# Performance work log

Measured on AMD Instinct MI355X. Metric: run time of the kernel, lower is better.

Reference implementation:

```python
import jax, jax.numpy as jnp
import numpy as np

TOTAL = 262144
NUM_SEG = 1024
H_DIM = 64
BF = 2  # block_flag_num
EPS = 1e-5


def setup_inputs() -> dict:
    key = jax.random.key(0)
    ks = jax.random.split(key, 12)
    # equal-length contiguous segments (ragged in general; equal here for setup)
    bounds = np.arange(0, TOTAL + 1, TOTAL // NUM_SEG, dtype=np.int64)
    seq_start_end = jnp.asarray(np.stack([bounds[:-1], bounds[1:]], axis=1))
    d_in = BF * 2          # 4
    d_emb = BF * 16        # 32
    d_pre = d_emb + H_DIM  # 96
    s = lambda n: 1.0 / np.sqrt(n)
    return {
        'h_state': jax.random.normal(ks[0], (TOTAL, H_DIM), jnp.float32),
        'end_block_pos_rel': jax.random.normal(ks[1], (TOTAL, 2, BF), jnp.float32),
        'W_sp': jax.random.normal(ks[2], (d_emb, d_in), jnp.float32) * s(d_in),
        'b_sp': jnp.zeros((d_emb,), jnp.float32),
        'W1': jax.random.normal(ks[3], (512, d_pre), jnp.float32) * s(d_pre),
        'b1': jnp.zeros((512,), jnp.float32),
        'g1': jnp.ones((512,), jnp.float32),
        'be1': jnp.zeros((512,), jnp.float32),
        'W2': jax.random.normal(ks[4], (1024, 512), jnp.float32) * s(512),
        'b2': jnp.zeros((1024,), jnp.float32),
        'g2': jnp.ones((1024,), jnp.float32),
        'be2': jnp.zeros((1024,), jnp.float32),
        'seq_start_end': seq_start_end,
    }


def _segment_bn(x, seg_ids, counts, gamma, beta):
    # training-mode BatchNorm1d computed independently per segment (biased var)
    num_seg = counts.shape[0]
    mean = jax.ops.segment_sum(x, seg_ids, num_segments=num_seg) / counts[:, None]
    ex2 = jax.ops.segment_sum(x * x, seg_ids, num_segments=num_seg) / counts[:, None]
    var = ex2 - mean * mean
    xn = (x - mean[seg_ids]) * jax.lax.rsqrt(var[seg_ids] + EPS)
    return xn * gamma + beta


def reference(h_state, end_block_pos_rel, W_sp, b_sp, W1, b1, g1, be1, W2, b2, g2, be2, seq_start_end):
    total = h_state.shape[0]
    starts = seq_start_end[:, 0]
    # contiguous segments: segment id of each row
    seg_ids = jnp.searchsorted(starts, jnp.arange(total), side='right') - 1
    counts = (seq_start_end[:, 1] - seq_start_end[:, 0]).astype(h_state.dtype)
    # permute(0,2,1).view(n,-1): (total, 2, BF) -> (total, BF*2)
    pos = jnp.transpose(end_block_pos_rel, (0, 2, 1)).reshape(total, -1)
    rel_emb = pos @ W_sp.T + b_sp                              # (total, 32)
    mlp_in = jnp.concatenate([rel_emb, h_state], axis=1)       # (total, 96)
    h1 = jax.nn.relu(_segment_bn(mlp_in @ W1.T + b1, seg_ids, counts, g1, be1))
    out = jax.nn.relu(_segment_bn(h1 @ W2.T + b2, seg_ids, counts, g2, be2))
    return out  # (total, 1024)
```

## Files before the change

kernel.cpp:

```cpp
#include <hip/hip_runtime.h>
#include <hip/hip_bf16.h>

#define TOTALROWS 262144
#define NSEG      1024
#define SEGROWS   256
#define HD        64
#define DEMB      32
#define DPRE      96
#define N1        512
#define N2        1024
#define EPSB      1e-5f

typedef short s16x8 __attribute__((ext_vector_type(8)));
typedef float f32x4 __attribute__((ext_vector_type(4)));

static __device__ __forceinline__ ushort f2bf(float x) {
    union { float f; unsigned u; } v; v.f = x;
    unsigned r = v.u + 0x7FFFu + ((v.u >> 16) & 1u);
    return (ushort)(r >> 16);
}

static __device__ __forceinline__ void gload_lds16(const void* g, void* l) {
    __builtin_amdgcn_global_load_lds(
        (const __attribute__((address_space(1))) void*)g,
        (__attribute__((address_space(3))) void*)l, 16, 0, 0);
}

__global__ void convert_w2_kernel(const float* __restrict__ w2, ushort* __restrict__ w2b) {
    int i = blockIdx.x * 256 + threadIdx.x;
    float4 v = ((const float4*)w2)[i];
    ushort4 o;
    o.x = f2bf(v.x); o.y = f2bf(v.y); o.z = f2bf(v.z); o.w = f2bf(v.w);
    ((ushort4*)w2b)[i] = o;
}

__global__ __launch_bounds__(512, 2) void layer1_kernel(
    const float* __restrict__ hstate, const float* __restrict__ ebpr,
    const float* __restrict__ Wsp, const float* __restrict__ W1,
    const float* __restrict__ g1, const float* __restrict__ be1,
    ushort* __restrict__ h1)
{
    __shared__ __align__(16) ushort As[SEGROWS * 104];
    __shared__ __align__(16) ushort Bs[SEGROWS * 104];
    __shared__ float statsS[8][4][16];
    __shared__ float statsQ[8][4][16];

    const int seg  = blockIdx.x;
    const int ct   = blockIdx.y;
    const int tid  = threadIdx.x;
    const int lane = tid & 63, wid = tid >> 6;
    const int wr   = wid >> 2, wc = wid & 3;

    {
        const float4* hs4 = (const float4*)(hstate + (size_t)seg * SEGROWS * HD);
        #pragma unroll
        for (int i = 0; i < 8; ++i) {
            int u = tid + i * 512;
            int r = u >> 4, c4 = u & 15;
            float4 v = hs4[u];
            ushort* dst = &As[r * 104 + DEMB + c4 * 4];
            dst[0] = f2bf(v.x); dst[1] = f2bf(v.y); dst[2] = f2bf(v.z); dst[3] = f2bf(v.w);
        }
        #pragma unroll
        for (int i = 0; i < 16; ++i) {
            int u = tid + i * 512;
            int r = u >> 5, k = u & 31;
            float4 e = ((const float4*)ebpr)[seg * SEGROWS + r];
            float4 w = ((const float4*)Wsp)[k];
            float val = w.x * e.x + w.y * e.z + w.z * e.y + w.w * e.w;
            As[r * 104 + k] = f2bf(val);
        }
    }
    {
        const float4* w14 = (const float4*)(W1 + (size_t)ct * 256 * DPRE);
        #pragma unroll
        for (int i = 0; i < 12; ++i) {
            int u = tid + i * 512;
            int r = u / 24, c4 = u % 24;
            float4 v = w14[u];
            ushort* dst = &Bs[r * 104 + c4 * 4];
            dst[0] = f2bf(v.x); dst[1] = f2bf(v.y); dst[2] = f2bf(v.z); dst[3] = f2bf(v.w);
        }
    }
    __syncthreads();

    f32x4 acc[8][4] = {};
    const int arow0 = wr * 128 + (lane & 15);
    const int bcol0 = wc * 64  + (lane & 15);
    const int kg    = (lane >> 4) * 8;
    #pragma unroll
    for (int ks = 0; ks < 3; ++ks) {
        s16x8 af[8], bfr[4];
        #pragma unroll
        for (int m = 0; m < 8; ++m)
            af[m] = *(const s16x8*)&As[(arow0 + m * 16) * 104 + ks * 32 + kg];
        #pragma unroll
        for (int n = 0; n < 4; ++n)
            bfr[n] = *(const s16x8*)&Bs[(bcol0 + n * 16) * 104 + ks * 32 + kg];
        #pragma unroll
        for (int m = 0; m < 8; ++m)
            #pragma unroll
            for (int n = 0; n < 4; ++n)
                acc[m][n] = __builtin_amdgcn_mfma_f32_16x16x32_bf16(af[m], bfr[n], acc[m][n], 0, 0, 0);
    }

    float s[4], q[4];
    #pragma unroll
    for (int n = 0; n < 4; ++n) { s[n] = 0.f; q[n] = 0.f; }
    #pragma unroll
    for (int m = 0; m < 8; ++m)
        #pragma unroll
        for (int n = 0; n < 4; ++n)
            #pragma unroll
            for (int j = 0; j < 4; ++j) { float v = acc[m][n][j]; s[n] += v; q[n] += v * v; }
    #pragma unroll
    for (int n = 0; n < 4; ++n) {
        s[n] += __shfl_xor(s[n], 16); q[n] += __shfl_xor(q[n], 16);
        s[n] += __shfl_xor(s[n], 32); q[n] += __shfl_xor(q[n], 32);
    }
    if ((lane >> 4) == 0) {
        #pragma unroll
        for (int n = 0; n < 4; ++n) { statsS[wid][n][lane] = s[n]; statsQ[wid][n][lane] = q[n]; }
    }
    __syncthreads();

    const float inv256 = 1.0f / 256.0f;
    float aa[4], bb[4];
    const int c16 = lane & 15;
    #pragma unroll
    for (int n = 0; n < 4; ++n) {
        float sum = statsS[wc][n][c16] + statsS[4 + wc][n][c16];
        float sq  = statsQ[wc][n][c16] + statsQ[4 + wc][n][c16];
        float mean = sum * inv256;
        float var  = sq * inv256 - mean * mean;
        float rinv = rsqrtf(var + EPSB);
        int col = ct * 256 + wc * 64 + n * 16 + c16;
        aa[n] = g1[col] * rinv;
        bb[n] = be1[col] - mean * aa[n];
    }

    ushort* outp = h1 + (size_t)(seg * SEGROWS) * N1 + ct * 256;
    const int rbase = wr * 128 + (lane >> 4) * 4;
    #pragma unroll
    for (int m = 0; m < 8; ++m)
        #pragma unroll
        for (int j = 0; j < 4; ++j) {
            int r = rbase + m * 16 + j;
            ushort* rowp = outp + (size_t)r * N1 + wc * 64 + c16;
            #pragma unroll
            for (int n = 0; n < 4; ++n) {
                float v = acc[m][n][j] * aa[n] + bb[n];
                v = v > 0.f ? v : 0.f;
                rowp[n * 16] = f2bf(v);
            }
        }
}


static __device__ __forceinline__ void stage_tile(
    const char* gA, const char* gB, char* lA, char* lB,
    int t, int wid, int lane)
{
    const int rsub = lane >> 2;
    const int cl   = (((lane & 3) ^ ((lane >> 3) & 3)) << 4);
    #pragma unroll
    for (int i = 0; i < 4; ++i) {
        int g = i * 4 + wid;
        gload_lds16(gA + (size_t)(g * 16 + rsub) * 1024 + (size_t)t * 64 + cl,
                    lA + g * 1024);
    }
    #pragma unroll
    for (int i = 0; i < 2; ++i) {
        int g = i * 4 + wid;
        gload_lds16(gB + (size_t)(g * 16 + rsub) * 1024 + (size_t)t * 64 + cl,
                    lB + g * 1024);
    }
}

static __device__ __forceinline__ void compute_step(
    const ushort* lA, const ushort* lB, f32x4 (&acc)[8][4],
    int arow0, int bcol0, int swz)
{
    s16x8 af[8], bfr[4];
    #pragma unroll
    for (int m = 0; m < 8; ++m)
        af[m] = *(const s16x8*)&lA[(arow0 + m * 16) * 32 + swz];
    #pragma unroll
    for (int n = 0; n < 4; ++n)
        bfr[n] = *(const s16x8*)&lB[(bcol0 + n * 16) * 32 + swz];
    __builtin_amdgcn_s_setprio(1);
    #pragma unroll
    for (int m = 0; m < 8; ++m)
        #pragma unroll
        for (int n = 0; n < 4; ++n)
            acc[m][n] = __builtin_amdgcn_mfma_f32_16x16x32_bf16(af[m], bfr[n], acc[m][n], 0, 0, 0);
    __builtin_amdgcn_s_setprio(0);
}

__global__ __launch_bounds__(256, 2) void layer2_kernel(
    const ushort* __restrict__ h1, const ushort* __restrict__ W2b,
    const float* __restrict__ g2, const float* __restrict__ be2,
    float* __restrict__ out)
{
    __shared__ __align__(16) ushort As[3][SEGROWS * 32];
    __shared__ __align__(16) ushort Bs[3][128 * 32];
    __shared__ float statsS[4][4][16];
    __shared__ float statsQ[4][4][16];

    const int b   = blockIdx.x;
    const int wg  = (b & 7) * 1024 + (b >> 3);
    const int seg = wg >> 3;
    const int ct  = wg & 7;

    const int tid  = threadIdx.x;
    const int lane = tid & 63, wid = tid >> 6;
    const int wr   = wid >> 1, wc = wid & 1;

    const char* srcA = (const char*)(h1  + (size_t)seg * SEGROWS * N1);
    const char* srcB = (const char*)(W2b + (size_t)ct  * 128    * N1);

    f32x4 acc[8][4] = {};
    const int arow0 = wr * 128 + (lane & 15);
    const int bcol0 = wc * 64  + (lane & 15);
    const int swz  = (((lane >> 4) ^ ((lane >> 1) & 3)) << 3);

    stage_tile(srcA, srcB, (char*)As[0], (char*)Bs[0], 0, wid, lane);
    stage_tile(srcA, srcB, (char*)As[1], (char*)Bs[1], 1, wid, lane);

#define L2_STEP(T, VW)                                                              \
    {                                                                               \
        if ((T) + 2 < 16)                                                           \
            stage_tile(srcA, srcB, (char*)As[((T)+2)%3], (char*)Bs[((T)+2)%3],      \
                       (T)+2, wid, lane);                                           \
        asm volatile("s_waitcnt vmcnt(" #VW ")" ::: "memory");                      \
        __builtin_amdgcn_s_barrier();                                               \
        compute_step(As[(T)%3], Bs[(T)%3], acc, arow0, bcol0, swz);                 \
        __builtin_amdgcn_s_barrier();                                               \
    }

    L2_STEP(0, 12)  L2_STEP(1, 12)  L2_STEP(2, 12)  L2_STEP(3, 12)
    L2_STEP(4, 12)  L2_STEP(5, 12)  L2_STEP(6, 12)  L2_STEP(7, 12)
    L2_STEP(8, 12)  L2_STEP(9, 12)  L2_STEP(10, 12) L2_STEP(11, 12)
    L2_STEP(12, 12) L2_STEP(13, 12) L2_STEP(14, 6)  L2_STEP(15, 0)
#undef L2_STEP

    float s[4], q[4];
    #pragma unroll
    for (int n = 0; n < 4; ++n) { s[n] = 0.f; q[n] = 0.f; }
    #pragma unroll
    for (int m = 0; m < 8; ++m)
        #pragma unroll
        for (int n = 0; n < 4; ++n)
            #pragma unroll
            for (int j = 0; j < 4; ++j) { float v = acc[m][n][j]; s[n] += v; q[n] += v * v; }
    #pragma unroll
    for (int n = 0; n < 4; ++n) {
        s[n] += __shfl_xor(s[n], 16); q[n] += __shfl_xor(q[n], 16);
        s[n] += __shfl_xor(s[n], 32); q[n] += __shfl_xor(q[n], 32);
    }
    if ((lane >> 4) == 0) {
        #pragma unroll
        for (int n = 0; n < 4; ++n) { statsS[wid][n][lane] = s[n]; statsQ[wid][n][lane] = q[n]; }
    }
    __syncthreads();

    const float inv256 = 1.0f / 256.0f;
    float aa[4], bb[4];
    const int c16 = lane & 15;
    #pragma unroll
    for (int n = 0; n < 4; ++n) {
        float sum = statsS[wc][n][c16] + statsS[2 + wc][n][c16];
        float sq  = statsQ[wc][n][c16] + statsQ[2 + wc][n][c16];
        float mean = sum * inv256;
        float var  = sq * inv256 - mean * mean;
        float rinv = rsqrtf(var + EPSB);
        int col = ct * 128 + wc * 64 + n * 16 + c16;
        aa[n] = g2[col] * rinv;
        bb[n] = be2[col] - mean * aa[n];
    }

    float* outp = out + (size_t)(seg * SEGROWS) * N2 + ct * 128;
    const int rbase = wr * 128 + (lane >> 4) * 4;
    #pragma unroll
    for (int m = 0; m < 8; ++m)
        #pragma unroll
        for (int j = 0; j < 4; ++j) {
            int r = rbase + m * 16 + j;
            float* rowp = outp + (size_t)r * N2 + wc * 64 + c16;
            #pragma unroll
            for (int n = 0; n < 4; ++n) {
                float v = acc[m][n][j] * aa[n] + bb[n];
                v = v > 0.f ? v : 0.f;
                __builtin_nontemporal_store(v, rowp + n * 16);
            }
        }
}

extern "C" void kernel_launch(void* const* d_in, const int* in_sizes, int n_in,
                              void* d_out, int out_size, void* d_ws, size_t ws_size,
                              hipStream_t stream) {
    const float* hstate = (const float*)d_in[0];
    const float* ebpr   = (const float*)d_in[1];
    const float* Wsp    = (const float*)d_in[2];
    const float* W1     = (const float*)d_in[4];
    const float* g1     = (const float*)d_in[6];
    const float* be1    = (const float*)d_in[7];
    const float* W2     = (const float*)d_in[8];
    const float* g2     = (const float*)d_in[10];
    const float* be2    = (const float*)d_in[11];
    float* outp         = (float*)d_out;

    ushort* h1  = (ushort*)d_ws;
    ushort* W2b = h1 + (size_t)TOTALROWS * N1;

    convert_w2_kernel<<<dim3((N2 * N1 / 4) / 256), dim3(256), 0, stream>>>(W2, W2b);
    layer1_kernel<<<dim3(NSEG, 2), dim3(512), 0, stream>>>(hstate, ebpr, Wsp, W1, g1, be1, h1);
    layer2_kernel<<<dim3(8192), dim3(256), 0, stream>>>(h1, W2b, g2, be2, outp);
}
```

Measured before the change: 646.3 us.

## Retile layer2 to 256x64 double-buffered tiles and merge layer1 column tiles

Layer2 now uses 256x64 output tiles with double buffering, occupancy 3, and regular stores in place of nontemporal ones. This doubles the grid and re-reads the h1 A tile twice as often. Layer1 now runs both column tiles in one block, reusing the staged activations, and reads W1 pre-converted to bf16 by an extended conversion kernel. Its activation staging uses vectorized LDS writes. The aim is better occupancy and less conversion and staging work, at the cost of more A-operand traffic in layer2.

```diff
diff --git a/kernel.cpp b/kernel.cpp
--- a/kernel.cpp
+++ b/kernel.cpp
@@ -12,6 +12,7 @@
 #define EPSB      1e-5f
 
 typedef short s16x8 __attribute__((ext_vector_type(8)));
+typedef short s16x4 __attribute__((ext_vector_type(4)));
 typedef float f32x4 __attribute__((ext_vector_type(4)));
 
 static __device__ __forceinline__ ushort f2bf(float x) {
@@ -26,17 +27,21 @@
         (__attribute__((address_space(3))) void*)l, 16, 0, 0);
 }
 
-__global__ void convert_w2_kernel(const float* __restrict__ w2, ushort* __restrict__ w2b) {
+__global__ void convert_w_kernel(const float* __restrict__ w2, ushort* __restrict__ w2b,
+                                 const float* __restrict__ w1, ushort* __restrict__ w1b) {
     int i = blockIdx.x * 256 + threadIdx.x;
-    float4 v = ((const float4*)w2)[i];
+    const float* src; ushort* dst; int j;
+    if (i < 131072) { src = w2; dst = w2b; j = i; }
+    else            { src = w1; dst = w1b; j = i - 131072; if (j >= 12288) return; }
+    float4 v = ((const float4*)src)[j];
     ushort4 o;
     o.x = f2bf(v.x); o.y = f2bf(v.y); o.z = f2bf(v.z); o.w = f2bf(v.w);
-    ((ushort4*)w2b)[i] = o;
+    ((ushort4*)dst)[j] = o;
 }
 
 __global__ __launch_bounds__(512, 2) void layer1_kernel(
     const float* __restrict__ hstate, const float* __restrict__ ebpr,
-    const float* __restrict__ Wsp, const float* __restrict__ W1,
+    const float* __restrict__ Wsp, const ushort* __restrict__ W1b,
     const float* __restrict__ g1, const float* __restrict__ be1,
     ushort* __restrict__ h1)
 {
@@ -46,7 +51,6 @@
     __shared__ float statsQ[8][4][16];
 
     const int seg  = blockIdx.x;
-    const int ct   = blockIdx.y;
     const int tid  = threadIdx.x;
     const int lane = tid & 63, wid = tid >> 6;
     const int wr   = wid >> 2, wc = wid & 3;
@@ -54,110 +58,125 @@
     {
         const float4* hs4 = (const float4*)(hstate + (size_t)seg * SEGROWS * HD);
         #pragma unroll
-        for (int i = 0; i < 8; ++i) {
+        for (int i = 0; i < 4; ++i) {
             int u = tid + i * 512;
-            int r = u >> 4, c4 = u & 15;
-            float4 v = hs4[u];
-            ushort* dst = &As[r * 104 + DEMB + c4 * 4];
-            dst[0] = f2bf(v.x); dst[1] = f2bf(v.y); dst[2] = f2bf(v.z); dst[3] = f2bf(v.w);
-        }
-        #pragma unroll
-        for (int i = 0; i < 16; ++i) {
+            int r = u >> 3, c8 = u & 7;
+            float4 v0 = hs4[2 * u];
+            float4 v1 = hs4[2 * u + 1];
+            s16x8 o;
+            o[0] = (short)f2bf(v0.x); o[1] = (short)f2bf(v0.y);
+            o[2] = (short)f2bf(v0.z); o[3] = (short)f2bf(v0.w);
+            o[4] = (short)f2bf(v1.x); o[5] = (short)f2bf(v1.y);
+            o[6] = (short)f2bf(v1.z); o[7] = (short)f2bf(v1.w);
+            *(s16x8*)&As[r * 104 + DEMB + c8 * 8] = o;
+        }
+    }
+    {
+        #pragma unroll
+        for (int i = 0; i < 4; ++i) {
             int u = tid + i * 512;
-            int r = u >> 5, k = u & 31;
+            int r = u >> 3, kq = u & 7;
             float4 e = ((const float4*)ebpr)[seg * SEGROWS + r];
-            float4 w = ((const float4*)Wsp)[k];
-            float val = w.x * e.x + w.y * e.z + w.z * e.y + w.w * e.w;
-            As[r * 104 + k] = f2bf(val);
-        }
-    }
-    {
-        const float4* w14 = (const float4*)(W1 + (size_t)ct * 256 * DPRE);
-        #pragma unroll
-        for (int i = 0; i < 12; ++i) {
-            int u = tid + i * 512;
-            int r = u / 24, c4 = u % 24;
-            float4 v = w14[u];
-            ushort* dst = &Bs[r * 104 + c4 * 4];
-            dst[0] = f2bf(v.x); dst[1] = f2bf(v.y); dst[2] = f2bf(v.z); dst[3] = f2bf(v.w);
-        }
-    }
-    __syncthreads();
-
-    f32x4 acc[8][4] = {};
-    const int arow0 = wr * 128 + (lane & 15);
-    const int bcol0 = wc * 64  + (lane & 15);
-    const int kg    = (lane >> 4) * 8;
-    #pragma unroll
-    for (int ks = 0; ks < 3; ++ks) {
-        s16x8 af[8], bfr[4];
+            s16x4 o;
+            #pragma unroll
+            for (int t = 0; t < 4; ++t) {
+                float4 w = ((const float4*)Wsp)[kq * 4 + t];
+                float val = w.x * e.x + w.y * e.z + w.z * e.y + w.w * e.w;
+                o[t] = (short)f2bf(val);
+            }
+            *(s16x4*)&As[r * 104 + kq * 4] = o;
+        }
+    }
+
+    #pragma unroll 1
+    for (int ct = 0; ct < 2; ++ct) {
+        {
+            const s16x8* w18 = (const s16x8*)(W1b + (size_t)ct * 256 * DPRE);
+            #pragma unroll
+            for (int i = 0; i < 6; ++i) {
+                int u = tid + i * 512;
+                int r = u / 12, c8 = u % 12;
+                *(s16x8*)&Bs[r * 104 + c8 * 8] = w18[u];
+            }
+        }
+        __syncthreads();
+
+        f32x4 acc[8][4] = {};
+        const int arow0 = wr * 128 + (lane & 15);
+        const int bcol0 = wc * 64  + (lane & 15);
+        const int kg    = (lane >> 4) * 8;
+        #pragma unroll
+        for (int ks = 0; ks < 3; ++ks) {
+            s16x8 af[8], bfr[4];
+            #pragma unroll
+            for (int m = 0; m < 8; ++m)
+                af[m] = *(const s16x8*)&As[(arow0 + m * 16) * 104 + ks * 32 + kg];
+            #pragma unroll
+            for (int n = 0; n < 4; ++n)
+                bfr[n] = *(const s16x8*)&Bs[(bcol0 + n * 16) * 104 + ks * 32 + kg];
+            #pragma unroll
+            for (int m = 0; m < 8; ++m)
+                #pragma unroll
+                for (int n = 0; n < 4; ++n)
+                    acc[m][n] = __builtin_amdgcn_mfma_f32_16x16x32_bf16(af[m], bfr[n], acc[m][n], 0, 0, 0);
+        }
+
+        float s[4], q[4];
+        #pragma unroll
+        for (int n = 0; n < 4; ++n) { s[n] = 0.f; q[n] = 0.f; }
         #pragma unroll
         for (int m = 0; m < 8; ++m)
-            af[m] = *(const s16x8*)&As[(arow0 + m * 16) * 104 + ks * 32 + kg];
-        #pragma unroll
-        for (int n = 0; n < 4; ++n)
-            bfr[n] = *(const s16x8*)&Bs[(bcol0 + n * 16) * 104 + ks * 32 + kg];
+            #pragma unroll
+            for (int n = 0; n < 4; ++n)
+                #pragma unroll
+                for (int j = 0; j < 4; ++j) { float v = acc[m][n][j]; s[n] += v; q[n] += v * v; }
+        #pragma unroll
+        for (int n = 0; n < 4; ++n) {
+            s[n] += __shfl_xor(s[n], 16); q[n] += __shfl_xor(q[n], 16);
+            s[n] += __shfl_xor(s[n], 32); q[n] += __shfl_xor(q[n], 32);
+        }
+        if ((lane >> 4) == 0) {
+            #pragma unroll
+            for (int n = 0; n < 4; ++n) { statsS[wid][n][lane] = s[n]; statsQ[wid][n][lane] = q[n]; }
+        }
+        __syncthreads();
+
+        const float inv256 = 1.0f / 256.0f;
+        float aa[4], bb[4];
+        const int c16 = lane & 15;
+        #pragma unroll
+        for (int n = 0; n < 4; ++n) {
+            float sum = statsS[wc][n][c16] + statsS[4 + wc][n][c16];
+            float sq  = statsQ[wc][n][c16] + statsQ[4 + wc][n][c16];
+            float mean = sum * inv256;
+            float var  = sq * inv256 - mean * mean;
+            float rinv = rsqrtf(var + EPSB);
+            int col = ct * 256 + wc * 64 + n * 16 + c16;
+            aa[n] = g1[col] * rinv;
+            bb[n] = be1[col] - mean * aa[n];
+        }
+
+        ushort* outp = h1 + (size_t)(seg * SEGROWS) * N1 + ct * 256;
+        const int rbase = wr * 128 + (lane >> 4) * 4;
         #pragma unroll
         for (int m = 0; m < 8; ++m)
             #pragma unroll
-            for (int n = 0; n < 4; ++n)
-                acc[m][n] = __builtin_amdgcn_mfma_f32_16x16x32_bf16(af[m], bfr[n], acc[m][n], 0, 0, 0);
-    }
-
-    float s[4], q[4];
-    #pragma unroll
-    for (int n = 0; n < 4; ++n) { s[n] = 0.f; q[n] = 0.f; }
-    #pragma unroll
-    for (int m = 0; m < 8; ++m)
-        #pragma unroll
-        for (int n = 0; n < 4; ++n)
-            #pragma unroll
-            for (int j = 0; j < 4; ++j) { float v = acc[m][n][j]; s[n] += v; q[n] += v * v; }
-    #pragma unroll
-    for (int n = 0; n < 4; ++n) {
-        s[n] += __shfl_xor(s[n], 16); q[n] += __shfl_xor(q[n], 16);
-        s[n] += __shfl_xor(s[n], 32); q[n] += __shfl_xor(q[n], 32);
-    }
-    if ((lane >> 4) == 0) {
-        #pragma unroll
-        for (int n = 0; n < 4; ++n) { statsS[wid][n][lane] = s[n]; statsQ[wid][n][lane] = q[n]; }
-    }
-    __syncthreads();
-
-    const float inv256 = 1.0f / 256.0f;
-    float aa[4], bb[4];
-    const int c16 = lane & 15;
-    #pragma unroll
-    for (int n = 0; n < 4; ++n) {
-        float sum = statsS[wc][n][c16] + statsS[4 + wc][n][c16];
-        float sq  = statsQ[wc][n][c16] + statsQ[4 + wc][n][c16];
-        float mean = sum * inv256;
-        float var  = sq * inv256 - mean * mean;
-        float rinv = rsqrtf(var + EPSB);
-        int col = ct * 256 + wc * 64 + n * 16 + c16;
-        aa[n] = g1[col] * rinv;
-        bb[n] = be1[col] - mean * aa[n];
-    }
-
-    ushort* outp = h1 + (size_t)(seg * SEGROWS) * N1 + ct * 256;
-    const int rbase = wr * 128 + (lane >> 4) * 4;
-    #pragma unroll
-    for (int m = 0; m < 8; ++m)
-        #pragma unroll
-        for (int j = 0; j < 4; ++j) {
-            int r = rbase + m * 16 + j;
-            ushort* rowp = outp + (size_t)r * N1 + wc * 64 + c16;
-            #pragma unroll
-            for (int n = 0; n < 4; ++n) {
-                float v = acc[m][n][j] * aa[n] + bb[n];
-                v = v > 0.f ? v : 0.f;
-                rowp[n * 16] = f2bf(v);
+            for (int j = 0; j < 4; ++j) {
+                int r = rbase + m * 16 + j;
+                ushort* rowp = outp + (size_t)r * N1 + wc * 64 + c16;
+                #pragma unroll
+                for (int n = 0; n < 4; ++n) {
+                    float v = acc[m][n][j] * aa[n] + bb[n];
+                    v = v > 0.f ? v : 0.f;
+                    rowp[n * 16] = f2bf(v);
+                }
             }
-        }
-}
-
-
-static __device__ __forceinline__ void stage_tile(
+        __syncthreads();
+    }
+}
+
+
+static __device__ __forceinline__ void stage_tile2(
     const char* gA, const char* gB, char* lA, char* lB,
     int t, int wid, int lane)
 {
@@ -169,86 +188,101 @@
         gload_lds16(gA + (size_t)(g * 16 + rsub) * 1024 + (size_t)t * 64 + cl,
                     lA + g * 1024);
     }
-    #pragma unroll
-    for (int i = 0; i < 2; ++i) {
-        int g = i * 4 + wid;
-        gload_lds16(gB + (size_t)(g * 16 + rsub) * 1024 + (size_t)t * 64 + cl,
-                    lB + g * 1024);
-    }
-}
-
-static __device__ __forceinline__ void compute_step(
-    const ushort* lA, const ushort* lB, f32x4 (&acc)[8][4],
+    gload_lds16(gB + (size_t)(wid * 16 + rsub) * 1024 + (size_t)t * 64 + cl,
+                lB + wid * 1024);
+}
+
+static __device__ __forceinline__ void compute_step2(
+    const ushort* lA, const ushort* lB, f32x4 (&acc)[4][4],
     int arow0, int bcol0, int swz)
 {
-    s16x8 af[8], bfr[4];
-    #pragma unroll
-    for (int m = 0; m < 8; ++m)
+    s16x8 af[4], bfr[4];
+    #pragma unroll
+    for (int m = 0; m < 4; ++m)
         af[m] = *(const s16x8*)&lA[(arow0 + m * 16) * 32 + swz];
     #pragma unroll
     for (int n = 0; n < 4; ++n)
         bfr[n] = *(const s16x8*)&lB[(bcol0 + n * 16) * 32 + swz];
     __builtin_amdgcn_s_setprio(1);
     #pragma unroll
-    for (int m = 0; m < 8; ++m)
+    for (int m = 0; m < 4; ++m)
         #pragma unroll
         for (int n = 0; n < 4; ++n)
             acc[m][n] = __builtin_amdgcn_mfma_f32_16x16x32_bf16(af[m], bfr[n], acc[m][n], 0, 0, 0);
     __builtin_amdgcn_s_setprio(0);
 }
 
-__global__ __launch_bounds__(256, 2) void layer2_kernel(
+__global__ __launch_bounds__(256, 3) void layer2_kernel(
     const ushort* __restrict__ h1, const ushort* __restrict__ W2b,
     const float* __restrict__ g2, const float* __restrict__ be2,
     float* __restrict__ out)
 {
-    __shared__ __align__(16) ushort As[3][SEGROWS * 32];
-    __shared__ __align__(16) ushort Bs[3][128 * 32];
+    __shared__ __align__(16) ushort As[2][SEGROWS * 32];
+    __shared__ __align__(16) ushort Bs[2][64 * 32];
     __shared__ float statsS[4][4][16];
     __shared__ float statsQ[4][4][16];
 
     const int b   = blockIdx.x;
-    const int wg  = (b & 7) * 1024 + (b >> 3);
-    const int seg = wg >> 3;
-    const int ct  = wg & 7;
+    const int wg  = (b & 7) * 2048 + (b >> 3);
+    const int seg = wg >> 4;
+    const int ct  = wg & 15;
 
     const int tid  = threadIdx.x;
     const int lane = tid & 63, wid = tid >> 6;
-    const int wr   = wid >> 1, wc = wid & 1;
+    const int wr   = wid;
 
     const char* srcA = (const char*)(h1  + (size_t)seg * SEGROWS * N1);
-    const char* srcB = (const char*)(W2b + (size_t)ct  * 128    * N1);
-
-    f32x4 acc[8][4] = {};
-    const int arow0 = wr * 128 + (lane & 15);
-    const int bcol0 = wc * 64  + (lane & 15);
-    const int swz  = (((lane >> 4) ^ ((lane >> 1) & 3)) << 3);
-
-    stage_tile(srcA, srcB, (char*)As[0], (char*)Bs[0], 0, wid, lane);
-    stage_tile(srcA, srcB, (char*)As[1], (char*)Bs[1], 1, wid, lane);
+    const char* srcB = (const char*)(W2b + (size_t)ct  * 64     * N1);
+
+    f32x4 acc[4][4] = {};
+    const int arow0 = wr * 64 + (lane & 15);
+    const int bcol0 = lane & 15;
+    const int swz   = (((lane >> 4) ^ ((lane >> 1) & 3)) << 3);
+
+    stage_tile2(srcA, srcB, (char*)As[0], (char*)Bs[0], 0, wid, lane);
+    stage_tile2(srcA, srcB, (char*)As[1], (char*)Bs[1], 1, wid, lane);
 
 #define L2_STEP(T, VW)                                                              \
     {                                                                               \
         if ((T) + 2 < 16)                                                           \
-            stage_tile(srcA, srcB, (char*)As[((T)+2)%3], (char*)Bs[((T)+2)%3],      \
-                       (T)+2, wid, lane);                                           \
+            stage_tile2(srcA, srcB, (char*)As[(T)&1], (char*)Bs[(T)&1],             \
+                        (T)+2, wid, lane);                                          \
         asm volatile("s_waitcnt vmcnt(" #VW ")" ::: "memory");                      \
-        __builtin_amdgcn_s_barrier();                                               \
-        compute_step(As[(T)%3], Bs[(T)%3], acc, arow0, bcol0, swz);                 \
-        __builtin_amdgcn_s_barrier();                                               \
-    }
-
-    L2_STEP(0, 12)  L2_STEP(1, 12)  L2_STEP(2, 12)  L2_STEP(3, 12)
-    L2_STEP(4, 12)  L2_STEP(5, 12)  L2_STEP(6, 12)  L2_STEP(7, 12)
-    L2_STEP(8, 12)  L2_STEP(9, 12)  L2_STEP(10, 12) L2_STEP(11, 12)
-    L2_STEP(12, 12) L2_STEP(13, 12) L2_STEP(14, 6)  L2_STEP(15, 0)
+        asm volatile("s_barrier" ::: "memory");                                     \
+        compute_step2(As[(T)&1], Bs[(T)&1], acc, arow0, bcol0, swz);                \
+        __builtin_amdgcn_sched_barrier(0);                                          \
+        asm volatile("s_barrier" ::: "memory");                                     \
+    }
 #undef L2_STEP
 
+#define L2_STEP(T, VW)                                                              \
+    {                                                                               \
+        if ((T) + 1 < 16)                                                           \
+            stage_tile2(srcA, srcB, (char*)As[((T)+1)&1], (char*)Bs[((T)+1)&1],     \
+                        (T)+1, wid, lane);                                          \
+        asm volatile("s_waitcnt vmcnt(" #VW ")" ::: "memory");                      \
+        asm volatile("s_barrier" ::: "memory");                                     \
+        compute_step2(As[(T)&1], Bs[(T)&1], acc, arow0, bcol0, swz);                \
+        __builtin_amdgcn_sched_barrier(0);                                          \
+        asm volatile("s_barrier" ::: "memory");                                     \
+    }
+    asm volatile("s_waitcnt vmcnt(5)" ::: "memory");
+    asm volatile("s_barrier" ::: "memory");
+    compute_step2(As[0], Bs[0], acc, arow0, bcol0, swz);
+    __builtin_amdgcn_sched_barrier(0);
+    asm volatile("s_barrier" ::: "memory");
+
+    L2_STEP(1, 5)   L2_STEP(2, 5)   L2_STEP(3, 5)
+    L2_STEP(4, 5)   L2_STEP(5, 5)   L2_STEP(6, 5)   L2_STEP(7, 5)
+    L2_STEP(8, 5)   L2_STEP(9, 5)   L2_STEP(10, 5)  L2_STEP(11, 5)
+    L2_STEP(12, 5)  L2_STEP(13, 5)  L2_STEP(14, 5)  L2_STEP(15, 0)
+#undef L2_STEP
+
     float s[4], q[4];
     #pragma unroll
     for (int n = 0; n < 4; ++n) { s[n] = 0.f; q[n] = 0.f; }
     #pragma unroll
-    for (int m = 0; m < 8; ++m)
+    for (int m = 0; m < 4; ++m)
         #pragma unroll
         for (int n = 0; n < 4; ++n)
             #pragma unroll
@@ -269,29 +303,31 @@
     const int c16 = lane & 15;
     #pragma unroll
     for (int n = 0; n < 4; ++n) {
-        float sum = statsS[wc][n][c16] + statsS[2 + wc][n][c16];
-        float sq  = statsQ[wc][n][c16] + statsQ[2 + wc][n][c16];
+        float sum = statsS[0][n][c16] + statsS[1][n][c16]
+                  + statsS[2][n][c16] + statsS[3][n][c16];
+        float sq  = statsQ[0][n][c16] + statsQ[1][n][c16]
+                  + statsQ[2][n][c16] + statsQ[3][n][c16];
         float mean = sum * inv256;
         float var  = sq * inv256 - mean * mean;
         float rinv = rsqrtf(var + EPSB);
-        int col = ct * 128 + wc * 64 + n * 16 + c16;
+        int col = ct * 64 + n * 16 + c16;
         aa[n] = g2[col] * rinv;
         bb[n] = be2[col] - mean * aa[n];
     }
 
-    float* outp = out + (size_t)(seg * SEGROWS) * N2 + ct * 128;
-    const int rbase = wr * 128 + (lane >> 4) * 4;
-    #pragma unroll
-    for (int m = 0; m < 8; ++m)
+    float* outp = out + (size_t)(seg * SEGROWS) * N2 + ct * 64;
+    const int rbase = wr * 64 + (lane >> 4) * 4;
+    #pragma unroll
+    for (int m = 0; m < 4; ++m)
         #pragma unroll
         for (int j = 0; j < 4; ++j) {
             int r = rbase + m * 16 + j;
-            float* rowp = outp + (size_t)r * N2 + wc * 64 + c16;
+            float* rowp = outp + (size_t)r * N2 + c16;
             #pragma unroll
             for (int n = 0; n < 4; ++n) {
                 float v = acc[m][n][j] * aa[n] + bb[n];
                 v = v > 0.f ? v : 0.f;
-                __builtin_nontemporal_store(v, rowp + n * 16);
+                rowp[n * 16] = v;
             }
         }
 }
@@ -312,8 +348,9 @@
 
     ushort* h1  = (ushort*)d_ws;
     ushort* W2b = h1 + (size_t)TOTALROWS * N1;
-
-    convert_w2_kernel<<<dim3((N2 * N1 / 4) / 256), dim3(256), 0, stream>>>(W2, W2b);
-    layer1_kernel<<<dim3(NSEG, 2), dim3(512), 0, stream>>>(hstate, ebpr, Wsp, W1, g1, be1, h1);
-    layer2_kernel<<<dim3(8192), dim3(256), 0, stream>>>(h1, W2b, g2, be2, outp);
-}
+    ushort* W1b = W2b + (size_t)N2 * N1;
+
+    convert_w_kernel<<<dim3(560), dim3(256), 0, stream>>>(W2, W2b, W1, W1b);
+    layer1_kernel<<<dim3(NSEG), dim3(512), 0, stream>>>(hstate, ebpr, Wsp, W1b, g1, be1, h1);
+    layer2_kernel<<<dim3(16384), dim3(256), 0, stream>>>(h1, W2b, g2, be2, outp);
+}
```

After: 695.4 us. 1.08x slower.
